# Optimization experiments

Measured on AMD Instinct MI355X. Metric: run time of the kernel, lower is better.

## Reference

```python
import jax, jax.numpy as jnp
import numpy as np
from jax import lax

B, M, N = 4096, 306, 984
LAMBDA = 0.1
MAX_ITER = 50


def setup_inputs() -> dict:
    key = jax.random.key(0)
    k1, k2, k3, k4 = jax.random.split(key, 4)
    return {
        "r_real": jax.random.normal(k1, (B, M), dtype=jnp.float32),
        "r_imag": jax.random.normal(k2, (B, M), dtype=jnp.float32),
        # phi buffer: torch.randn(M, N, dtype=complex64) -> real/imag each ~N(0, 1/2)?
        # torch.randn(complex64) draws real & imag each from N(0, 1/sqrt(2)^2)=N(0,0.5).
        "phi_real": jax.random.normal(k3, (M, N), dtype=jnp.float32) * np.float32(1.0 / np.sqrt(2.0)),
        "phi_imag": jax.random.normal(k4, (M, N), dtype=jnp.float32) * np.float32(1.0 / np.sqrt(2.0)),
    }


def reference(r_real, r_imag, phi_real, phi_imag):
    phi = (phi_real + 1j * phi_imag).astype(jnp.complex64)          # [M, N]
    r = (r_real + 1j * r_imag).astype(jnp.complex64)                # [B, M]
    # step_size = 1 / ||phi||_2^2  (spectral norm squared)
    step = (1.0 / jnp.linalg.norm(phi, ord=2) ** 2).real.astype(jnp.float32)
    thresh = (LAMBDA * step).astype(jnp.float32)
    phi_c = jnp.conj(phi)

    def body(w, _):
        # error = w @ phi.T - r : [B, M]
        error = jnp.einsum("bn,mn->bm", w, phi) - r
        # gradient = error @ conj(phi) : [B, N]
        grad = jnp.einsum("bm,mn->bn", error, phi_c)
        w_next = w - step * grad
        w_mag = jnp.abs(w_next)
        new_mag = jax.nn.relu(w_mag - thresh)
        # polar(new_mag, angle(w_next))
        w_new = (new_mag * jnp.exp(1j * jnp.angle(w_next))).astype(jnp.complex64)
        return w_new, None

    w0 = jnp.zeros((r.shape[0], N), dtype=jnp.complex64)
    w, _ = lax.scan(body, w0, None, length=MAX_ITER)
    return jnp.abs(w).astype(jnp.float32)
```

## Files before the change

### kernel.cpp

```cpp
#include <hip/hip_runtime.h>
#include <math.h>

#define Bb 4096
#define Mm 306
#define Nn 984
#define NCP 1024
#define KA 2048
#define ITERS 50
#define KSQ 9

typedef _Float16 f16x8 __attribute__((ext_vector_type(8)));
typedef float f32x16 __attribute__((ext_vector_type(16)));

__device__ __forceinline__ void cmac(float2& c, const float2 a, const float2 b) {
    c.x = fmaf(a.x, b.x, c.x);
    c.x = fmaf(-a.y, b.y, c.x);
    c.y = fmaf(a.x, b.y, c.y);
    c.y = fmaf(a.y, b.x, c.y);
}

__device__ __forceinline__ unsigned short f16bits(float v) {
    union { _Float16 h; unsigned short u; } cv;
    cv.h = (_Float16)v;
    return cv.u;
}
__device__ __forceinline__ float f16lo(unsigned int u) {
    union { unsigned short s; _Float16 h; } cv; cv.s = (unsigned short)(u & 0xffffu);
    return (float)cv.h;
}
__device__ __forceinline__ float f16hi(unsigned int u) {
    union { unsigned short s; _Float16 h; } cv; cv.s = (unsigned short)(u >> 16);
    return (float)cv.h;
}

__device__ __forceinline__ void load_lds16(const void* g, void* l) {
    __builtin_amdgcn_global_load_lds((const __attribute__((address_space(1))) void*)g,
                                     (__attribute__((address_space(3))) void*)l, 16, 0, 0);
}

__device__ __forceinline__ size_t swzA(int b, int c) {
    return ((size_t)(((b >> 7) * 32 + (c >> 5)) * 1024 + ((c >> 2) & 7) * 128 + (b & 127))) * 4 + (c & 3);
}
__device__ __forceinline__ size_t swzB(int jr, int q) {
    return ((size_t)(((jr >> 7) * 32 + (q >> 5)) * 1024 + ((q >> 2) & 7) * 128 + (jr & 127))) * 4 + (q & 3);
}

__global__ void gram_kernel(const float* __restrict__ pr, const float* __restrict__ pi,
                            float2* __restrict__ G) {
    int j = blockIdx.x * 16 + threadIdx.x;
    int i = blockIdx.y * 16 + threadIdx.y;
    if (i >= Mm || j >= Mm) return;
    const float* pri = pr + (size_t)i * Nn;
    const float* pii = pi + (size_t)i * Nn;
    const float* prj = pr + (size_t)j * Nn;
    const float* pij = pi + (size_t)j * Nn;
    float ar = 0.f, ai = 0.f;
    for (int n = 0; n < Nn; ++n) {
        float xr = pri[n], xi = pii[n], yr = prj[n], yi = pij[n];
        ar = fmaf(xr, yr, ar); ar = fmaf(xi, yi, ar);
        ai = fmaf(xi, yr, ai); ai = fmaf(-xr, yi, ai);
    }
    G[i * Mm + j] = make_float2(ar, ai);
}

__global__ void frob_kernel(const float2* __restrict__ H, float* __restrict__ slot, int n) {
    int idx = blockIdx.x * blockDim.x + threadIdx.x;
    int stride = gridDim.x * blockDim.x;
    float s = 0.f;
    for (int i = idx; i < n; i += stride) {
        float2 v = H[i];
        s = fmaf(v.x, v.x, s);
        s = fmaf(v.y, v.y, s);
    }
    #pragma unroll
    for (int o = 32; o > 0; o >>= 1) s += __shfl_down(s, o, 64);
    __shared__ float wsum[4];
    int lane = threadIdx.x & 63, wv = threadIdx.x >> 6;
    if (lane == 0) wsum[wv] = s;
    __syncthreads();
    if (threadIdx.x == 0) atomicAdd(slot, wsum[0] + wsum[1] + wsum[2] + wsum[3]);
}

__global__ void sqmm_kernel(const float2* __restrict__ A, float2* __restrict__ C,
                            const float* __restrict__ fslot) {
    __shared__ float2 As[32][33];
    __shared__ float2 Bs[32][33];
    float inv = 1.0f / fslot[0];
    int tx = threadIdx.x, ty = threadIdx.y;
    int t = ty * 16 + tx;
    int r0 = blockIdx.y * 32, c0 = blockIdx.x * 32;
    int zs = blockIdx.z * 80;
    int ze = zs + 80 < Mm ? zs + 80 : Mm;
    float2 acc[2][2] = {};
    for (int k0 = zs; k0 < ze; k0 += 32) {
        #pragma unroll
        for (int i = 0; i < 4; ++i) {
            int idx = t + i * 256;
            int rr = idx >> 5, cc = idx & 31;
            int gr = r0 + rr, gk = k0 + cc;
            As[rr][cc] = (gr < Mm && gk < ze) ? A[gr * Mm + gk] : make_float2(0.f, 0.f);
            int gk2 = k0 + rr, gc = c0 + cc;
            Bs[rr][cc] = (gk2 < ze && gc < Mm) ? A[gk2 * Mm + gc] : make_float2(0.f, 0.f);
        }
        __syncthreads();
        #pragma unroll 8
        for (int kk = 0; kk < 32; ++kk) {
            float2 a0 = As[ty * 2][kk], a1 = As[ty * 2 + 1][kk];
            float2 b0 = Bs[kk][tx * 2], b1 = Bs[kk][tx * 2 + 1];
            cmac(acc[0][0], a0, b0); cmac(acc[0][1], a0, b1);
            cmac(acc[1][0], a1, b0); cmac(acc[1][1], a1, b1);
        }
        __syncthreads();
    }
    #pragma unroll
    for (int i = 0; i < 2; ++i) {
        int gr = r0 + ty * 2 + i;
        #pragma unroll
        for (int j = 0; j < 2; ++j) {
            int gc = c0 + tx * 2 + j;
            if (gr < Mm && gc < Mm) {
                atomicAdd(&C[gr * Mm + gc].x, acc[i][j].x * inv);
                atomicAdd(&C[gr * Mm + gc].y, acc[i][j].y * inv);
            }
        }
    }
}

__global__ void rayleigh_kernel(const float2* __restrict__ H, const float2* __restrict__ G,
                                float* __restrict__ sc) {
    __shared__ float2 v[Mm];
    __shared__ float rn[320], rd[320];
    int t = threadIdx.x;
    if (t < Mm) {
        float2 s = make_float2(0.f, 0.f);
        for (int j = 0; j < Mm; ++j) { float2 h = H[t * Mm + j]; s.x += h.x; s.y += h.y; }
        v[t] = s;
    }
    __syncthreads();
    float num = 0.f, den = 0.f;
    if (t < Mm) {
        float2 u = make_float2(0.f, 0.f);
        for (int k = 0; k < Mm; ++k) {
            float2 g = G[k * Mm + t];
            float2 vk = v[k];
            u.x = fmaf(g.x, vk.x, u.x); u.x = fmaf(g.y, vk.y, u.x);
            u.y = fmaf(g.x, vk.y, u.y); u.y = fmaf(-g.y, vk.x, u.y);
        }
        float2 vt = v[t];
        num = vt.x * u.x + vt.y * u.y;
        den = vt.x * vt.x + vt.y * vt.y;
    }
    rn[t] = num; rd[t] = den;
    __syncthreads();
    if (t == 0) {
        float sn = 0.f, sd = 0.f;
        for (int i = 0; i < 320; ++i) { sn += rn[i]; sd += rd[i]; }
        float lam = sn / sd;
        float step = 1.0f / lam;
        sc[0] = step;
        sc[1] = 0.1f * step;
    }
}

__global__ void qpack_kernel(const float* __restrict__ pr, const float* __restrict__ pi,
                             unsigned int* __restrict__ Bu, const float* __restrict__ sc) {
    __shared__ float2 Pn[16][33];
    __shared__ float2 Pc[16][33];
    float nstep = -sc[0];
    int t = threadIdx.x;
    int tx = t & 15, ty = t >> 4;
    int n0 = blockIdx.x * 32, c0 = blockIdx.y * 32;
    float2 q[2][2] = {};
    for (int m0 = 0; m0 < Mm; m0 += 16) {
        #pragma unroll
        for (int rep = 0; rep < 2; ++rep) {
            int idx = t + rep * 256;
            int mm = idx >> 5, col = idx & 31;
            int gm = m0 + mm;
            float2 a = make_float2(0.f, 0.f), b = make_float2(0.f, 0.f);
            if (gm < Mm) {
                if (n0 + col < Nn) a = make_float2(pr[(size_t)gm * Nn + n0 + col], pi[(size_t)gm * Nn + n0 + col]);
                if (c0 + col < Nn) b = make_float2(pr[(size_t)gm * Nn + c0 + col], pi[(size_t)gm * Nn + c0 + col]);
            }
            Pn[mm][col] = a; Pc[mm][col] = b;
        }
        __syncthreads();
        #pragma unroll
        for (int mm = 0; mm < 16; ++mm) {
            float2 a0 = Pn[mm][ty * 2], a1 = Pn[mm][ty * 2 + 1];
            float2 b0 = Pc[mm][tx * 2], b1 = Pc[mm][tx * 2 + 1];
            #define QMAC(qq, aa, bb) \
                qq.x = fmaf(aa.x, bb.x, qq.x); qq.x = fmaf(aa.y, bb.y, qq.x); \
                qq.y = fmaf(aa.y, bb.x, qq.y); qq.y = fmaf(-aa.x, bb.y, qq.y);
            QMAC(q[0][0], a0, b0) QMAC(q[0][1], a0, b1)
            QMAC(q[1][0], a1, b0) QMAC(q[1][1], a1, b1)
            #undef QMAC
        }
        __syncthreads();
    }
    #pragma unroll
    for (int i = 0; i < 2; ++i) {
        int n = n0 + ty * 2 + i;
        #pragma unroll
        for (int j = 0; j < 2; ++j) {
            int c = c0 + tx * 2 + j;
            if (n < Nn && c < Nn) {
                float MR = nstep * q[i][j].x, MI = nstep * q[i][j].y;
                unsigned short hR = f16bits(MR);
                unsigned short hI = f16bits(MI);
                unsigned short nhI = hI ^ 0x8000u;
                int jr = ((c >> 5) * 64) + (c & 31);
                Bu[swzB(jr, n)]      = (unsigned)hR | ((unsigned)nhI << 16);
                Bu[swzB(jr + 32, n)] = (unsigned)hI | ((unsigned)hR << 16);
            }
        }
    }
}

__global__ __launch_bounds__(256) void rphi_kernel(
    const float* __restrict__ rr, const float* __restrict__ ri,
    const float* __restrict__ pr, const float* __restrict__ pi,
    unsigned int* __restrict__ rph16, const float* __restrict__ sc) {
    __shared__ float2 As[64][18];
    __shared__ float2 Bs[16][66];
    float step = sc[0];
    int t = threadIdx.x;
    int tx = t & 15, ty = t >> 4;
    int b0 = blockIdx.x * 64, c0 = blockIdx.y * 64;
    float2 acc[4][4] = {};
    for (int k0 = 0; k0 < Mm; k0 += 16) {
        #pragma unroll
        for (int rep = 0; rep < 4; ++rep) {
            int idx = t + rep * 256;
            int row = idx >> 4, kk = idx & 15;
            int gk = k0 + kk;
            float re = 0.f, im = 0.f;
            if (gk < Mm) {
                re = rr[(size_t)(b0 + row) * Mm + gk];
                im = ri[(size_t)(b0 + row) * Mm + gk];
            }
            As[row][kk] = make_float2(re, im);
        }
        {
            int rb = t >> 4, sb = t & 15;
            int gm = k0 + rb, gc = c0 + sb * 4;
            float4 vr = make_float4(0.f, 0.f, 0.f, 0.f), vi = vr;
            if (gm < Mm && gc < Nn) {
                vr = *reinterpret_cast<const float4*>(&pr[(size_t)gm * Nn + gc]);
                vi = *reinterpret_cast<const float4*>(&pi[(size_t)gm * Nn + gc]);
            }
            Bs[rb][sb * 4 + 0] = make_float2(vr.x, -vi.x);
            Bs[rb][sb * 4 + 1] = make_float2(vr.y, -vi.y);
            Bs[rb][sb * 4 + 2] = make_float2(vr.z, -vi.z);
            Bs[rb][sb * 4 + 3] = make_float2(vr.w, -vi.w);
        }
        __syncthreads();
        #pragma unroll
        for (int kk = 0; kk < 16; ++kk) {
            float2 a[4], b[4];
            #pragma unroll
            for (int i = 0; i < 4; ++i) a[i] = As[ty * 4 + i][kk];
            #pragma unroll
            for (int j = 0; j < 4; ++j) b[j] = Bs[kk][tx * 4 + j];
            #pragma unroll
            for (int i = 0; i < 4; ++i)
                #pragma unroll
                for (int j = 0; j < 4; ++j) cmac(acc[i][j], a[i], b[j]);
        }
        __syncthreads();
    }
    #pragma unroll
    for (int i = 0; i < 4; ++i) {
        int gb = b0 + ty * 4 + i;
        #pragma unroll
        for (int j = 0; j < 4; ++j) {
            int gc = c0 + tx * 4 + j;
            rph16[(size_t)gb * NCP + gc] =
                (unsigned)f16bits(step * acc[i][j].x) | ((unsigned)f16bits(step * acc[i][j].y) << 16);
        }
    }
}

__global__ __launch_bounds__(256, 2) void ista7_kernel(
    const _Float16* __restrict__ wfi, const _Float16* __restrict__ Bq,
    unsigned int* __restrict__ wfo,
    const unsigned int* __restrict__ rph16,
    const float* __restrict__ sc, float* __restrict__ out, int last) {
    __shared__ _Float16 As[8192];
    __shared__ _Float16 Bs[8192];
    int tid = threadIdx.x;
    int lane = tid & 63, wv = tid >> 6;
    int wm = wv & 1, wn = wv >> 1;
    int bblk = blockIdx.x, nblk = blockIdx.y;
    int l31 = lane & 31, lh = lane >> 5;

    f32x16 acc[2][2] = {};

    for (int kt = 0; kt < 32; ++kt) {
        #pragma unroll
        for (int c = 0; c < 4; ++c) {
            int u = c * 256 + tid;
            const char* ga = (const char*)wfi + (((size_t)(bblk * 32 + kt)) * 1024 + u) * 16;
            load_lds16(ga, &As[(size_t)(c * 256 + wv * 64) * 8]);
            const char* gb = (const char*)Bq + (((size_t)(nblk * 32 + kt)) * 1024 + u) * 16;
            load_lds16(gb, &Bs[(size_t)(c * 256 + wv * 64) * 8]);
        }
        __syncthreads();
        #pragma unroll
        for (int s = 0; s < 4; ++s) {
            int kq = s * 2 + lh;
            f16x8 af[2], bfr[2];
            #pragma unroll
            for (int mt = 0; mt < 2; ++mt)
                af[mt] = *reinterpret_cast<const f16x8*>(
                    &As[(size_t)(kq * 128 + wm * 64 + mt * 32 + l31) * 8]);
            #pragma unroll
            for (int nt = 0; nt < 2; ++nt)
                bfr[nt] = *reinterpret_cast<const f16x8*>(
                    &Bs[(size_t)(kq * 128 + wn * 64 + nt * 32 + l31) * 8]);
            #pragma unroll
            for (int mt = 0; mt < 2; ++mt)
                #pragma unroll
                for (int nt = 0; nt < 2; ++nt)
                    acc[mt][nt] = __builtin_amdgcn_mfma_f32_32x32x16_f16(af[mt], bfr[nt], acc[mt][nt], 0, 0, 0);
        }
        __syncthreads();
    }

    float thr = sc[1];
    int b0 = bblk * 128;
    int c = nblk * 64 + wn * 32 + l31;
    const unsigned int* wfin = (const unsigned int*)wfi;
    #pragma unroll
    for (int mt = 0; mt < 2; ++mt) {
        #pragma unroll
        for (int reg = 0; reg < 16; ++reg) {
            int row = b0 + wm * 64 + mt * 32 + ((reg & 3) + 8 * (reg >> 2) + 4 * lh);
            unsigned int wu = wfin[swzA(row, c)];
            unsigned int ru = rph16[(size_t)row * NCP + c];
            float zr = f16lo(wu) + acc[mt][0][reg] + f16lo(ru);
            float zi = f16hi(wu) + acc[mt][1][reg] + f16hi(ru);
            float mag = sqrtf(zr * zr + zi * zi);
            float nm = mag - thr;
            float f = (nm > 0.f) ? (nm / mag) : 0.f;
            float orr = zr * f, oii = zi * f;
            wfo[swzA(row, c)] = (unsigned)f16bits(orr) | ((unsigned)f16bits(oii) << 16);
            if (last && c < Nn) out[(size_t)row * Nn + c] = fmaxf(nm, 0.f);
        }
    }
}

extern "C" void kernel_launch(void* const* d_in, const int* in_sizes, int n_in,
                              void* d_out, int out_size, void* d_ws, size_t ws_size,
                              hipStream_t stream) {
    const float* rr = (const float*)d_in[0];
    const float* ri = (const float*)d_in[1];
    const float* pr = (const float*)d_in[2];
    const float* pi = (const float*)d_in[3];
    float* out = (float*)d_out;

    char* ws = (char*)d_ws;
    size_t off = 0;
    _Float16* wf0 = (_Float16*)(ws + off); off += (size_t)Bb * KA * sizeof(_Float16);
    _Float16* wf1 = (_Float16*)(ws + off); off += (size_t)Bb * KA * sizeof(_Float16);
    _Float16* Bq  = (_Float16*)(ws + off); off += (size_t)2048 * 2048 * sizeof(_Float16);
    unsigned int* rph16 = (unsigned int*)(ws + off); off += (size_t)Bb * NCP * 4;
    float2* G = (float2*)(ws + off);     off += (size_t)Mm * Mm * sizeof(float2);
    float2* H1 = (float2*)(ws + off);    off += (size_t)Mm * Mm * sizeof(float2);
    float2* H2 = (float2*)(ws + off);    off += (size_t)Mm * Mm * sizeof(float2);
    float* slots = (float*)(ws + off);   off += 64 * sizeof(float);
    float* sc = slots + 32;

    (void)hipMemsetAsync(wf0, 0, (size_t)Bb * KA * sizeof(_Float16), stream);
    (void)hipMemsetAsync(Bq, 0, (size_t)2048 * 2048 * sizeof(_Float16), stream);
    (void)hipMemsetAsync(slots, 0, 64 * sizeof(float), stream);

    gram_kernel<<<dim3(20, 20), dim3(16, 16), 0, stream>>>(pr, pi, G);
    float2* bufs[2] = { H1, H2 };
    const float2* src = G;
    for (int s = 0; s < KSQ; ++s) {
        frob_kernel<<<128, 256, 0, stream>>>(src, slots + s, Mm * Mm);
        float2* dst = bufs[s & 1];
        (void)hipMemsetAsync(dst, 0, (size_t)Mm * Mm * sizeof(float2), stream);
        sqmm_kernel<<<dim3(10, 10, 4), dim3(16, 16), 0, stream>>>(src, dst, slots + s);
        src = dst;
    }
    rayleigh_kernel<<<1, 320, 0, stream>>>(src, G, sc);

    qpack_kernel<<<dim3(31, 31), 256, 0, stream>>>(pr, pi, (unsigned int*)Bq, sc);
    rphi_kernel<<<dim3(64, 16), 256, 0, stream>>>(rr, ri, pr, pi, rph16, sc);

    _Float16* wbuf[2] = { wf0, wf1 };
    for (int it = 0; it < ITERS; ++it) {
        ista7_kernel<<<dim3(32, 16), 256, 0, stream>>>(
            wbuf[it & 1], Bq, (unsigned int*)wbuf[(it + 1) & 1], rph16, sc, out,
            it == ITERS - 1 ? 1 : 0);
    }
}
```

Measured before the change: 3.184 ms.

## Replace precomputed NxN Gram GEMM with two thin GEMMs through M

Drops the precomputed I - step·PhiᴴPhi (984x984, padded to 2048 in K) operator. Each iteration now runs two GEMMs: w·Phiᵀ into an fp16 error buffer (K=2048, output padded to 640), then error·conj(Phi) with K=640 plus the shrinkage epilogue. Per-iteration MFMA work drops because both inner dimensions pass through M=306 instead of N=984. The cost is an extra kernel launch per iteration, an fp16 round-trip of the intermediate error, and a different rounding path.

```diff
diff --git a/kernel.cpp b/kernel.cpp
--- a/kernel.cpp
+++ b/kernel.cpp
@@ -43,6 +43,12 @@
 }
 __device__ __forceinline__ size_t swzB(int jr, int q) {
     return ((size_t)(((jr >> 7) * 32 + (q >> 5)) * 1024 + ((q >> 2) & 7) * 128 + (jr & 127))) * 4 + (q & 3);
+}
+__device__ __forceinline__ size_t swzA2(int b, int c) {
+    return ((size_t)(((b >> 7) * 10 + (c >> 5)) * 1024 + ((c >> 2) & 7) * 128 + (b & 127))) * 4 + (c & 3);
+}
+__device__ __forceinline__ size_t swzB2(int jr, int q) {
+    return ((size_t)(((jr >> 7) * 10 + (q >> 5)) * 1024 + ((q >> 2) & 7) * 128 + (jr & 127))) * 4 + (q & 3);
 }
 
 __global__ void gram_kernel(const float* __restrict__ pr, const float* __restrict__ pi,
@@ -162,59 +168,22 @@
     }
 }
 
-__global__ void qpack_kernel(const float* __restrict__ pr, const float* __restrict__ pi,
-                             unsigned int* __restrict__ Bu, const float* __restrict__ sc) {
-    __shared__ float2 Pn[16][33];
-    __shared__ float2 Pc[16][33];
-    float nstep = -sc[0];
-    int t = threadIdx.x;
-    int tx = t & 15, ty = t >> 4;
-    int n0 = blockIdx.x * 32, c0 = blockIdx.y * 32;
-    float2 q[2][2] = {};
-    for (int m0 = 0; m0 < Mm; m0 += 16) {
-        #pragma unroll
-        for (int rep = 0; rep < 2; ++rep) {
-            int idx = t + rep * 256;
-            int mm = idx >> 5, col = idx & 31;
-            int gm = m0 + mm;
-            float2 a = make_float2(0.f, 0.f), b = make_float2(0.f, 0.f);
-            if (gm < Mm) {
-                if (n0 + col < Nn) a = make_float2(pr[(size_t)gm * Nn + n0 + col], pi[(size_t)gm * Nn + n0 + col]);
-                if (c0 + col < Nn) b = make_float2(pr[(size_t)gm * Nn + c0 + col], pi[(size_t)gm * Nn + c0 + col]);
-            }
-            Pn[mm][col] = a; Pc[mm][col] = b;
-        }
-        __syncthreads();
-        #pragma unroll
-        for (int mm = 0; mm < 16; ++mm) {
-            float2 a0 = Pn[mm][ty * 2], a1 = Pn[mm][ty * 2 + 1];
-            float2 b0 = Pc[mm][tx * 2], b1 = Pc[mm][tx * 2 + 1];
-            #define QMAC(qq, aa, bb) \
-                qq.x = fmaf(aa.x, bb.x, qq.x); qq.x = fmaf(aa.y, bb.y, qq.x); \
-                qq.y = fmaf(aa.y, bb.x, qq.y); qq.y = fmaf(-aa.x, bb.y, qq.y);
-            QMAC(q[0][0], a0, b0) QMAC(q[0][1], a0, b1)
-            QMAC(q[1][0], a1, b0) QMAC(q[1][1], a1, b1)
-            #undef QMAC
-        }
-        __syncthreads();
-    }
-    #pragma unroll
-    for (int i = 0; i < 2; ++i) {
-        int n = n0 + ty * 2 + i;
-        #pragma unroll
-        for (int j = 0; j < 2; ++j) {
-            int c = c0 + tx * 2 + j;
-            if (n < Nn && c < Nn) {
-                float MR = nstep * q[i][j].x, MI = nstep * q[i][j].y;
-                unsigned short hR = f16bits(MR);
-                unsigned short hI = f16bits(MI);
-                unsigned short nhI = hI ^ 0x8000u;
-                int jr = ((c >> 5) * 64) + (c & 31);
-                Bu[swzB(jr, n)]      = (unsigned)hR | ((unsigned)nhI << 16);
-                Bu[swzB(jr + 32, n)] = (unsigned)hI | ((unsigned)hR << 16);
-            }
-        }
-    }
+__global__ void ppack_kernel(const float* __restrict__ pr, const float* __restrict__ pi,
+                             unsigned int* __restrict__ B1u, unsigned int* __restrict__ B2u,
+                             const float* __restrict__ sc) {
+    int n = blockIdx.x * 256 + threadIdx.x;
+    int m = blockIdx.y;
+    if (n >= Nn) return;
+    float xr = pr[(size_t)m * Nn + n], xi = pi[(size_t)m * Nn + n];
+    unsigned short a = f16bits(xr), b = f16bits(xi);
+    int jr1 = ((m >> 5) * 64) + (m & 31);
+    B1u[swzB(jr1, n)]      = (unsigned)a | ((unsigned)(b ^ 0x8000u) << 16);
+    B1u[swzB(jr1 + 32, n)] = (unsigned)b | ((unsigned)a << 16);
+    float s = sc[0];
+    unsigned short x = f16bits(-s * xr), y = f16bits(-s * xi);
+    int jr2 = ((n >> 5) * 64) + (n & 31);
+    B2u[swzB2(jr2, m)]      = (unsigned)x | ((unsigned)y << 16);
+    B2u[swzB2(jr2 + 32, m)] = (unsigned)(y ^ 0x8000u) | ((unsigned)x << 16);
 }
 
 __global__ __launch_bounds__(256) void rphi_kernel(
@@ -281,9 +250,66 @@
     }
 }
 
-__global__ __launch_bounds__(256, 2) void ista7_kernel(
-    const _Float16* __restrict__ wfi, const _Float16* __restrict__ Bq,
-    unsigned int* __restrict__ wfo,
+__global__ __launch_bounds__(256, 2) void gemm_e_kernel(
+    const _Float16* __restrict__ wfi, const _Float16* __restrict__ B1,
+    unsigned int* __restrict__ errU) {
+    __shared__ _Float16 As[8192];
+    __shared__ _Float16 Bs[8192];
+    int tid = threadIdx.x;
+    int lane = tid & 63, wv = tid >> 6;
+    int wm = wv & 1, wn = wv >> 1;
+    int bblk = blockIdx.x, nblk = blockIdx.y;
+    int l31 = lane & 31, lh = lane >> 5;
+
+    f32x16 acc[2][2] = {};
+
+    for (int kt = 0; kt < 32; ++kt) {
+        #pragma unroll
+        for (int c = 0; c < 4; ++c) {
+            int u = c * 256 + tid;
+            const char* ga = (const char*)wfi + (((size_t)(bblk * 32 + kt)) * 1024 + u) * 16;
+            load_lds16(ga, &As[(size_t)(c * 256 + wv * 64) * 8]);
+            const char* gb = (const char*)B1 + (((size_t)(nblk * 32 + kt)) * 1024 + u) * 16;
+            load_lds16(gb, &Bs[(size_t)(c * 256 + wv * 64) * 8]);
+        }
+        __syncthreads();
+        #pragma unroll
+        for (int s = 0; s < 4; ++s) {
+            int kq = s * 2 + lh;
+            f16x8 af[2], bfr[2];
+            #pragma unroll
+            for (int mt = 0; mt < 2; ++mt)
+                af[mt] = *reinterpret_cast<const f16x8*>(
+                    &As[(size_t)(kq * 128 + wm * 64 + mt * 32 + l31) * 8]);
+            #pragma unroll
+            for (int nt = 0; nt < 2; ++nt)
+                bfr[nt] = *reinterpret_cast<const f16x8*>(
+                    &Bs[(size_t)(kq * 128 + wn * 64 + nt * 32 + l31) * 8]);
+            #pragma unroll
+            for (int mt = 0; mt < 2; ++mt)
+                #pragma unroll
+                for (int nt = 0; nt < 2; ++nt)
+                    acc[mt][nt] = __builtin_amdgcn_mfma_f32_32x32x16_f16(af[mt], bfr[nt], acc[mt][nt], 0, 0, 0);
+        }
+        __syncthreads();
+    }
+
+    int b0 = bblk * 128;
+    int c = nblk * 64 + wn * 32 + l31;
+    #pragma unroll
+    for (int mt = 0; mt < 2; ++mt) {
+        #pragma unroll
+        for (int reg = 0; reg < 16; ++reg) {
+            int row = b0 + wm * 64 + mt * 32 + ((reg & 3) + 8 * (reg >> 2) + 4 * lh);
+            errU[swzA2(row, c)] =
+                (unsigned)f16bits(acc[mt][0][reg]) | ((unsigned)f16bits(acc[mt][1][reg]) << 16);
+        }
+    }
+}
+
+__global__ __launch_bounds__(256, 2) void gemm_w_kernel(
+    const _Float16* __restrict__ errF, const _Float16* __restrict__ B2,
+    const _Float16* __restrict__ wfi, unsigned int* __restrict__ wfo,
     const unsigned int* __restrict__ rph16,
     const float* __restrict__ sc, float* __restrict__ out, int last) {
     __shared__ _Float16 As[8192];
@@ -296,13 +322,13 @@
 
     f32x16 acc[2][2] = {};
 
-    for (int kt = 0; kt < 32; ++kt) {
+    for (int kt = 0; kt < 10; ++kt) {
         #pragma unroll
         for (int c = 0; c < 4; ++c) {
             int u = c * 256 + tid;
-            const char* ga = (const char*)wfi + (((size_t)(bblk * 32 + kt)) * 1024 + u) * 16;
+            const char* ga = (const char*)errF + (((size_t)(bblk * 10 + kt)) * 1024 + u) * 16;
             load_lds16(ga, &As[(size_t)(c * 256 + wv * 64) * 8]);
-            const char* gb = (const char*)Bq + (((size_t)(nblk * 32 + kt)) * 1024 + u) * 16;
+            const char* gb = (const char*)B2 + (((size_t)(nblk * 10 + kt)) * 1024 + u) * 16;
             load_lds16(gb, &Bs[(size_t)(c * 256 + wv * 64) * 8]);
         }
         __syncthreads();
@@ -343,8 +369,7 @@
             float mag = sqrtf(zr * zr + zi * zi);
             float nm = mag - thr;
             float f = (nm > 0.f) ? (nm / mag) : 0.f;
-            float orr = zr * f, oii = zi * f;
-            wfo[swzA(row, c)] = (unsigned)f16bits(orr) | ((unsigned)f16bits(oii) << 16);
+            wfo[swzA(row, c)] = (unsigned)f16bits(zr * f) | ((unsigned)f16bits(zi * f) << 16);
             if (last && c < Nn) out[(size_t)row * Nn + c] = fmaxf(nm, 0.f);
         }
     }
@@ -363,7 +388,9 @@
     size_t off = 0;
     _Float16* wf0 = (_Float16*)(ws + off); off += (size_t)Bb * KA * sizeof(_Float16);
     _Float16* wf1 = (_Float16*)(ws + off); off += (size_t)Bb * KA * sizeof(_Float16);
-    _Float16* Bq  = (_Float16*)(ws + off); off += (size_t)2048 * 2048 * sizeof(_Float16);
+    _Float16* B1  = (_Float16*)(ws + off); off += (size_t)640 * 2048 * sizeof(_Float16);
+    _Float16* B2  = (_Float16*)(ws + off); off += (size_t)2048 * 640 * sizeof(_Float16);
+    _Float16* errF = (_Float16*)(ws + off); off += (size_t)Bb * 640 * sizeof(_Float16);
     unsigned int* rph16 = (unsigned int*)(ws + off); off += (size_t)Bb * NCP * 4;
     float2* G = (float2*)(ws + off);     off += (size_t)Mm * Mm * sizeof(float2);
     float2* H1 = (float2*)(ws + off);    off += (size_t)Mm * Mm * sizeof(float2);
@@ -372,7 +399,8 @@
     float* sc = slots + 32;
 
     (void)hipMemsetAsync(wf0, 0, (size_t)Bb * KA * sizeof(_Float16), stream);
-    (void)hipMemsetAsync(Bq, 0, (size_t)2048 * 2048 * sizeof(_Float16), stream);
+    (void)hipMemsetAsync(B1, 0, (size_t)640 * 2048 * sizeof(_Float16), stream);
+    (void)hipMemsetAsync(B2, 0, (size_t)2048 * 640 * sizeof(_Float16), stream);
     (void)hipMemsetAsync(slots, 0, 64 * sizeof(float), stream);
 
     gram_kernel<<<dim3(20, 20), dim3(16, 16), 0, stream>>>(pr, pi, G);
@@ -387,13 +415,16 @@
     }
     rayleigh_kernel<<<1, 320, 0, stream>>>(src, G, sc);
 
-    qpack_kernel<<<dim3(31, 31), 256, 0, stream>>>(pr, pi, (unsigned int*)Bq, sc);
+    ppack_kernel<<<dim3((Nn + 255) / 256, Mm), 256, 0, stream>>>(
+        pr, pi, (unsigned int*)B1, (unsigned int*)B2, sc);
     rphi_kernel<<<dim3(64, 16), 256, 0, stream>>>(rr, ri, pr, pi, rph16, sc);
 
     _Float16* wbuf[2] = { wf0, wf1 };
     for (int it = 0; it < ITERS; ++it) {
-        ista7_kernel<<<dim3(32, 16), 256, 0, stream>>>(
-            wbuf[it & 1], Bq, (unsigned int*)wbuf[(it + 1) & 1], rph16, sc, out,
+        gemm_e_kernel<<<dim3(32, 5), 256, 0, stream>>>(
+            wbuf[it & 1], B1, (unsigned int*)errF);
+        gemm_w_kernel<<<dim3(32, 16), 256, 0, stream>>>(
+            errF, B2, wbuf[it & 1], (unsigned int*)wbuf[(it + 1) & 1], rph16, sc, out,
             it == ITERS - 1 ? 1 : 0);
     }
 }
```

New measurement: 3.574 ms. 12.2% more time.

## Compute r·conj(phi) with fp16 MFMA and flatten ISTA grid indexing

Applied to the files above, without the earlier changes.

Replaces the scalar fp32 complex GEMM that computes step*r·conj(phi) with packing kernels that convert r and -step*phi into swizzled fp16 tiles, followed by an MFMA-based GEMM that reuses the ISTA kernel's tiling. The ISTA launch also changes from a 2D grid to a 1D grid with bblk/nblk decoded so that consecutive blocks share a b-tile. This removes the slow one-time FP32 FMA GEMM at the cost of extra pack launches, memsets and fp16 rounding of the r and phi inputs.

```diff
diff --git a/kernel.cpp b/kernel.cpp
--- a/kernel.cpp
+++ b/kernel.cpp
@@ -43,6 +43,12 @@
 }
 __device__ __forceinline__ size_t swzB(int jr, int q) {
     return ((size_t)(((jr >> 7) * 32 + (q >> 5)) * 1024 + ((q >> 2) & 7) * 128 + (jr & 127))) * 4 + (q & 3);
+}
+__device__ __forceinline__ size_t swzA2(int b, int c) {
+    return ((size_t)(((b >> 7) * 10 + (c >> 5)) * 1024 + ((c >> 2) & 7) * 128 + (b & 127))) * 4 + (c & 3);
+}
+__device__ __forceinline__ size_t swzB2(int jr, int q) {
+    return ((size_t)(((jr >> 7) * 10 + (q >> 5)) * 1024 + ((q >> 2) & 7) * 128 + (jr & 127))) * 4 + (q & 3);
 }
 
 __global__ void gram_kernel(const float* __restrict__ pr, const float* __restrict__ pi,
@@ -217,66 +223,80 @@
     }
 }
 
-__global__ __launch_bounds__(256) void rphi_kernel(
-    const float* __restrict__ rr, const float* __restrict__ ri,
-    const float* __restrict__ pr, const float* __restrict__ pi,
-    unsigned int* __restrict__ rph16, const float* __restrict__ sc) {
-    __shared__ float2 As[64][18];
-    __shared__ float2 Bs[16][66];
-    float step = sc[0];
-    int t = threadIdx.x;
-    int tx = t & 15, ty = t >> 4;
-    int b0 = blockIdx.x * 64, c0 = blockIdx.y * 64;
-    float2 acc[4][4] = {};
-    for (int k0 = 0; k0 < Mm; k0 += 16) {
-        #pragma unroll
-        for (int rep = 0; rep < 4; ++rep) {
-            int idx = t + rep * 256;
-            int row = idx >> 4, kk = idx & 15;
-            int gk = k0 + kk;
-            float re = 0.f, im = 0.f;
-            if (gk < Mm) {
-                re = rr[(size_t)(b0 + row) * Mm + gk];
-                im = ri[(size_t)(b0 + row) * Mm + gk];
-            }
-            As[row][kk] = make_float2(re, im);
-        }
-        {
-            int rb = t >> 4, sb = t & 15;
-            int gm = k0 + rb, gc = c0 + sb * 4;
-            float4 vr = make_float4(0.f, 0.f, 0.f, 0.f), vi = vr;
-            if (gm < Mm && gc < Nn) {
-                vr = *reinterpret_cast<const float4*>(&pr[(size_t)gm * Nn + gc]);
-                vi = *reinterpret_cast<const float4*>(&pi[(size_t)gm * Nn + gc]);
-            }
-            Bs[rb][sb * 4 + 0] = make_float2(vr.x, -vi.x);
-            Bs[rb][sb * 4 + 1] = make_float2(vr.y, -vi.y);
-            Bs[rb][sb * 4 + 2] = make_float2(vr.z, -vi.z);
-            Bs[rb][sb * 4 + 3] = make_float2(vr.w, -vi.w);
-        }
-        __syncthreads();
-        #pragma unroll
-        for (int kk = 0; kk < 16; ++kk) {
-            float2 a[4], b[4];
-            #pragma unroll
-            for (int i = 0; i < 4; ++i) a[i] = As[ty * 4 + i][kk];
-            #pragma unroll
-            for (int j = 0; j < 4; ++j) b[j] = Bs[kk][tx * 4 + j];
-            #pragma unroll
-            for (int i = 0; i < 4; ++i)
+__global__ void rpack_kernel(const float* __restrict__ rr, const float* __restrict__ ri,
+                             unsigned int* __restrict__ rp16) {
+    int b = blockIdx.x * 256 + threadIdx.x;
+    int m = blockIdx.y;
+    rp16[swzA2(b, m)] = (unsigned)f16bits(rr[(size_t)b * Mm + m]) |
+                        ((unsigned)f16bits(ri[(size_t)b * Mm + m]) << 16);
+}
+
+__global__ void ppack2_kernel(const float* __restrict__ pr, const float* __restrict__ pi,
+                              unsigned int* __restrict__ B2u, const float* __restrict__ sc) {
+    int n = blockIdx.x * 256 + threadIdx.x;
+    int m = blockIdx.y;
+    if (n >= Nn) return;
+    float s = sc[0];
+    float xr = pr[(size_t)m * Nn + n], xi = pi[(size_t)m * Nn + n];
+    unsigned short x = f16bits(-s * xr), y = f16bits(-s * xi);
+    int jr2 = ((n >> 5) * 64) + (n & 31);
+    B2u[swzB2(jr2, m)]      = (unsigned)x | ((unsigned)y << 16);
+    B2u[swzB2(jr2 + 32, m)] = (unsigned)(y ^ 0x8000u) | ((unsigned)x << 16);
+}
+
+__global__ __launch_bounds__(256, 2) void rphi_mfma_kernel(
+    const _Float16* __restrict__ rp16, const _Float16* __restrict__ B2,
+    unsigned int* __restrict__ rph16) {
+    __shared__ _Float16 As[8192];
+    __shared__ _Float16 Bs[8192];
+    int tid = threadIdx.x;
+    int lane = tid & 63, wv = tid >> 6;
+    int wm = wv & 1, wn = wv >> 1;
+    int bblk = blockIdx.x, nblk = blockIdx.y;
+    int l31 = lane & 31, lh = lane >> 5;
+
+    f32x16 acc[2][2] = {};
+
+    for (int kt = 0; kt < 10; ++kt) {
+        #pragma unroll
+        for (int c = 0; c < 4; ++c) {
+            int u = c * 256 + tid;
+            const char* ga = (const char*)rp16 + (((size_t)(bblk * 10 + kt)) * 1024 + u) * 16;
+            load_lds16(ga, &As[(size_t)(c * 256 + wv * 64) * 8]);
+            const char* gb = (const char*)B2 + (((size_t)(nblk * 10 + kt)) * 1024 + u) * 16;
+            load_lds16(gb, &Bs[(size_t)(c * 256 + wv * 64) * 8]);
+        }
+        __syncthreads();
+        #pragma unroll
+        for (int s = 0; s < 4; ++s) {
+            int kq = s * 2 + lh;
+            f16x8 af[2], bfr[2];
+            #pragma unroll
+            for (int mt = 0; mt < 2; ++mt)
+                af[mt] = *reinterpret_cast<const f16x8*>(
+                    &As[(size_t)(kq * 128 + wm * 64 + mt * 32 + l31) * 8]);
+            #pragma unroll
+            for (int nt = 0; nt < 2; ++nt)
+                bfr[nt] = *reinterpret_cast<const f16x8*>(
+                    &Bs[(size_t)(kq * 128 + wn * 64 + nt * 32 + l31) * 8]);
+            #pragma unroll
+            for (int mt = 0; mt < 2; ++mt)
                 #pragma unroll
-                for (int j = 0; j < 4; ++j) cmac(acc[i][j], a[i], b[j]);
-        }
-        __syncthreads();
-    }
+                for (int nt = 0; nt < 2; ++nt)
+                    acc[mt][nt] = __builtin_amdgcn_mfma_f32_32x32x16_f16(af[mt], bfr[nt], acc[mt][nt], 0, 0, 0);
+        }
+        __syncthreads();
+    }
+
+    int b0 = bblk * 128;
+    int c = nblk * 64 + wn * 32 + l31;
     #pragma unroll
-    for (int i = 0; i < 4; ++i) {
-        int gb = b0 + ty * 4 + i;
-        #pragma unroll
-        for (int j = 0; j < 4; ++j) {
-            int gc = c0 + tx * 4 + j;
-            rph16[(size_t)gb * NCP + gc] =
-                (unsigned)f16bits(step * acc[i][j].x) | ((unsigned)f16bits(step * acc[i][j].y) << 16);
+    for (int mt = 0; mt < 2; ++mt) {
+        #pragma unroll
+        for (int reg = 0; reg < 16; ++reg) {
+            int row = b0 + wm * 64 + mt * 32 + ((reg & 3) + 8 * (reg >> 2) + 4 * lh);
+            rph16[(size_t)row * NCP + c] =
+                (unsigned)f16bits(-acc[mt][0][reg]) | ((unsigned)f16bits(-acc[mt][1][reg]) << 16);
         }
     }
 }
@@ -291,7 +311,9 @@
     int tid = threadIdx.x;
     int lane = tid & 63, wv = tid >> 6;
     int wm = wv & 1, wn = wv >> 1;
-    int bblk = blockIdx.x, nblk = blockIdx.y;
+    int id = blockIdx.x;
+    int bblk = id >> 4;
+    int nblk = id & 15;
     int l31 = lane & 31, lh = lane >> 5;
 
     f32x16 acc[2][2] = {};
@@ -343,8 +365,7 @@
             float mag = sqrtf(zr * zr + zi * zi);
             float nm = mag - thr;
             float f = (nm > 0.f) ? (nm / mag) : 0.f;
-            float orr = zr * f, oii = zi * f;
-            wfo[swzA(row, c)] = (unsigned)f16bits(orr) | ((unsigned)f16bits(oii) << 16);
+            wfo[swzA(row, c)] = (unsigned)f16bits(zr * f) | ((unsigned)f16bits(zi * f) << 16);
             if (last && c < Nn) out[(size_t)row * Nn + c] = fmaxf(nm, 0.f);
         }
     }
@@ -365,6 +386,8 @@
     _Float16* wf1 = (_Float16*)(ws + off); off += (size_t)Bb * KA * sizeof(_Float16);
     _Float16* Bq  = (_Float16*)(ws + off); off += (size_t)2048 * 2048 * sizeof(_Float16);
     unsigned int* rph16 = (unsigned int*)(ws + off); off += (size_t)Bb * NCP * 4;
+    _Float16* rp16 = (_Float16*)(ws + off); off += (size_t)Bb * 640 * sizeof(_Float16);
+    _Float16* B2  = (_Float16*)(ws + off); off += (size_t)2048 * 640 * sizeof(_Float16);
     float2* G = (float2*)(ws + off);     off += (size_t)Mm * Mm * sizeof(float2);
     float2* H1 = (float2*)(ws + off);    off += (size_t)Mm * Mm * sizeof(float2);
     float2* H2 = (float2*)(ws + off);    off += (size_t)Mm * Mm * sizeof(float2);
@@ -373,6 +396,8 @@
 
     (void)hipMemsetAsync(wf0, 0, (size_t)Bb * KA * sizeof(_Float16), stream);
     (void)hipMemsetAsync(Bq, 0, (size_t)2048 * 2048 * sizeof(_Float16), stream);
+    (void)hipMemsetAsync(rp16, 0, (size_t)Bb * 640 * sizeof(_Float16), stream);
+    (void)hipMemsetAsync(B2, 0, (size_t)2048 * 640 * sizeof(_Float16), stream);
     (void)hipMemsetAsync(slots, 0, 64 * sizeof(float), stream);
 
     gram_kernel<<<dim3(20, 20), dim3(16, 16), 0, stream>>>(pr, pi, G);
@@ -388,11 +413,13 @@
     rayleigh_kernel<<<1, 320, 0, stream>>>(src, G, sc);
 
     qpack_kernel<<<dim3(31, 31), 256, 0, stream>>>(pr, pi, (unsigned int*)Bq, sc);
-    rphi_kernel<<<dim3(64, 16), 256, 0, stream>>>(rr, ri, pr, pi, rph16, sc);
+    rpack_kernel<<<dim3(16, Mm), 256, 0, stream>>>(rr, ri, (unsigned int*)rp16);
+    ppack2_kernel<<<dim3(4, Mm), 256, 0, stream>>>(pr, pi, (unsigned int*)B2, sc);
+    rphi_mfma_kernel<<<dim3(32, 16), 256, 0, stream>>>(rp16, B2, rph16);
 
     _Float16* wbuf[2] = { wf0, wf1 };
     for (int it = 0; it < ITERS; ++it) {
-        ista7_kernel<<<dim3(32, 16), 256, 0, stream>>>(
+        ista7_kernel<<<512, 256, 0, stream>>>(
             wbuf[it & 1], Bq, (unsigned int*)wbuf[(it + 1) & 1], rph16, sc, out,
             it == ITERS - 1 ? 1 : 0);
     }
```

After: 3.106 ms. 2.4% less time.
